# Optimization experiments

Hardware: AMD Instinct MI355X
Metric: run time of the kernel (lower is better)

The kernel has to match this reference:

```python
import jax, jax.numpy as jnp
import numpy as np

B, L, D_MODEL, H, D_QKV = 4, 2048, 1024, 16, 64
SCALE = float(D_MODEL) ** 0.5  # note: source scales by sqrt(d_model), not sqrt(d_qkv)


def setup_inputs() -> dict:
    key = jax.random.key(0)
    ks = jax.random.split(key, 6)
    xavier_qkv = (2.0 / (D_MODEL + D_QKV)) ** 0.5
    xavier_fc = (2.0 / (H * D_QKV + D_MODEL)) ** 0.5
    return {
        "x": jax.random.normal(ks[0], (B, L, D_MODEL), dtype=jnp.float32),
        "mask": jnp.ones((B, L), dtype=jnp.int32),
        "w_q": jax.random.normal(ks[1], (H, D_MODEL, D_QKV), dtype=jnp.float32) * xavier_qkv,
        "w_k": jax.random.normal(ks[2], (H, D_MODEL, D_QKV), dtype=jnp.float32) * xavier_qkv,
        "w_v": jax.random.normal(ks[3], (H, D_MODEL, D_QKV), dtype=jnp.float32) * xavier_qkv,
        "fc_w": jax.random.normal(ks[4], (D_MODEL, H * D_QKV), dtype=jnp.float32) * xavier_fc,
        "fc_b": jnp.zeros((D_MODEL,), dtype=jnp.float32),
    }


def reference(x, mask, w_q, w_k, w_v, fc_w, fc_b):
    # x: [B, L, M]; per-head projections via einsum, as in the source
    q = jnp.einsum('blm,hmd->blhd', x, w_q)
    k = jnp.einsum('blm,hmd->blhd', x, w_k)
    v = jnp.einsum('blm,hmd->blhd', x, w_v)
    scores = jnp.einsum('blhd,bkhd->bhlk', q, k)  # [B, H, L, L]
    m = mask[:, None, None, :]  # unsqueeze(1).unsqueeze(2)
    scores = jnp.where(m == 0, jnp.asarray(-1e9, scores.dtype), scores)
    logits = jax.nn.softmax(scores / SCALE, axis=3)
    # Faithful to source einsum 'bhlk,blhd->blhd' (k is summed out of logits only)
    out = jnp.einsum('bhlk,blhd->blhd', logits, v)
    out = out.reshape(x.shape[0], x.shape[1], H * D_QKV)
    return out @ fc_w.T + fc_b
```

## Files before the change

kernel.cpp:

```cpp
#include <hip/hip_runtime.h>
#include <hip/hip_bf16.h>


typedef __attribute__((ext_vector_type(8))) short bf16x8;
typedef __attribute__((ext_vector_type(4))) float f32x4;

__device__ __forceinline__ f32x4 mfma16(bf16x8 a, bf16x8 b, f32x4 c) {
  return __builtin_amdgcn_mfma_f32_16x16x32_bf16(a, b, c, 0, 0, 0);
}

__device__ __forceinline__ unsigned short f2b(float f) {
  unsigned int u = __builtin_bit_cast(unsigned int, f);
  return (unsigned short)((u + 0x7fffu + ((u >> 16) & 1u)) >> 16);
}

__device__ __forceinline__ bf16x8 cvt8(float4 a, float4 b) {
  bf16x8 r;
  r[0] = (short)f2b(a.x); r[1] = (short)f2b(a.y); r[2] = (short)f2b(a.z); r[3] = (short)f2b(a.w);
  r[4] = (short)f2b(b.x); r[5] = (short)f2b(b.y); r[6] = (short)f2b(b.z); r[7] = (short)f2b(b.w);
  return r;
}

__device__ __forceinline__ void gld_lds16(const void* g, void* l) {
  __builtin_amdgcn_global_load_lds((const __attribute__((address_space(1))) unsigned int*)g,
                                   (__attribute__((address_space(3))) unsigned int*)l, 16, 0, 0);
}

__global__ void cast8(const float* __restrict__ in, unsigned short* __restrict__ out) {
  int i = (blockIdx.x * 256 + threadIdx.x) * 8;
  float4 a = *reinterpret_cast<const float4*>(in + i);
  float4 b = *reinterpret_cast<const float4*>(in + i + 4);
  *reinterpret_cast<bf16x8*>(out + i) = cvt8(a, b);
}

__global__ __launch_bounds__(512) void fold_w(const float* __restrict__ fcw,
                                              const float* __restrict__ wv,
                                              unsigned short* __restrict__ wcT) {
  int wid = threadIdx.x >> 6, lane = threadIdx.x & 63, l16 = lane & 15, quad = lane >> 4;
  int wk = wid >> 2, wr = (wid >> 1) & 1, wc = wid & 1;
  int row0 = blockIdx.y * 64 + wr * 32;
  int col0 = blockIdx.x * 64 + wc * 32;
  f32x4 acc[2][2];
#pragma unroll
  for (int a = 0; a < 2; a++)
#pragma unroll
    for (int b = 0; b < 2; b++) acc[a][b] = (f32x4){0.f, 0.f, 0.f, 0.f};

  for (int k0 = wk * 512; k0 < wk * 512 + 512; k0 += 32) {
    int kk = k0 + quad * 8;
    int h = kk >> 6, d = kk & 63;
    bf16x8 af[2], bfr[2];
#pragma unroll
    for (int rt = 0; rt < 2; rt++) {
      const float* pa = fcw + (row0 + rt * 16 + l16) * 1024 + kk;
      af[rt] = cvt8(*reinterpret_cast<const float4*>(pa), *reinterpret_cast<const float4*>(pa + 4));
    }
#pragma unroll
    for (int ct = 0; ct < 2; ct++) {
      const float* pb = wv + h * 65536 + (col0 + ct * 16 + l16) * 64 + d;
      bfr[ct] = cvt8(*reinterpret_cast<const float4*>(pb), *reinterpret_cast<const float4*>(pb + 4));
    }
#pragma unroll
    for (int rt = 0; rt < 2; rt++)
#pragma unroll
      for (int ct = 0; ct < 2; ct++) acc[rt][ct] = mfma16(af[rt], bfr[ct], acc[rt][ct]);
  }

  __shared__ f32x4 red[4][64][4];
  if (wk == 1) {
#pragma unroll
    for (int rt = 0; rt < 2; rt++)
#pragma unroll
      for (int ct = 0; ct < 2; ct++) red[wid & 3][lane][rt * 2 + ct] = acc[rt][ct];
  }
  __syncthreads();
  if (wk == 0) {
#pragma unroll
    for (int rt = 0; rt < 2; rt++)
#pragma unroll
      for (int ct = 0; ct < 2; ct++) {
        f32x4 s = acc[rt][ct];
        f32x4 o = red[wid & 3][lane][rt * 2 + ct];
        int j0 = row0 + rt * 16 + quad * 4;
        int m = col0 + ct * 16 + l16;
#pragma unroll
        for (int r = 0; r < 4; r++) wcT[(j0 + r) * 1024 + m] = f2b(s[r] + o[r]);
      }
  }
}

__global__ __launch_bounds__(256) void final_gemm(const unsigned short* __restrict__ xb,
                                                  const unsigned short* __restrict__ wcT,
                                                  const float* __restrict__ fcb,
                                                  float* __restrict__ out) {
  __shared__ __align__(16) unsigned short As[2 * 128 * 32];
  __shared__ __align__(16) unsigned short Bs[2 * 128 * 32];
  int t = threadIdx.x, wid = t >> 6, lane = t & 63, l16 = lane & 15, quad = lane >> 4;
  int wr = wid >> 1, wc = wid & 1;
  int row0 = blockIdx.x * 128;
  int col0 = blockIdx.y * 128;

  int w4 = wid * 4;
  const unsigned short* Ap[4];
  const unsigned short* Bp[4];
#pragma unroll
  for (int j = 0; j < 4; j++) {
    int blk = w4 + j;
    int s = blk >> 3, r0 = (blk & 7) * 16;
    int row = r0 + (lane >> 2), kq = lane & 3;
    Ap[j] = xb + (row0 + row) * 1024 + s * 32 + kq * 8;
    Bp[j] = wcT + (col0 + row) * 1024 + s * 32 + kq * 8;
  }

  f32x4 acc[16];
#pragma unroll
  for (int i = 0; i < 16; i++) acc[i] = (f32x4){0.f, 0.f, 0.f, 0.f};

  for (int k0 = 0; k0 < 1024; k0 += 64) {
    __syncthreads();
#pragma unroll
    for (int j = 0; j < 4; j++) {
      int off = (w4 + j) * 512 + lane * 8;
      gld_lds16(Ap[j] + k0, &As[off]);
      gld_lds16(Bp[j] + k0, &Bs[off]);
    }
    __syncthreads();

#pragma unroll
    for (int s = 0; s < 2; s++) {
      bf16x8 af[4], bfr[4];
#pragma unroll
      for (int rt = 0; rt < 4; rt++)
        af[rt] = *reinterpret_cast<const bf16x8*>(&As[s * 4096 + (wr * 64 + rt * 16 + l16) * 32 + quad * 8]);
#pragma unroll
      for (int ct = 0; ct < 4; ct++)
        bfr[ct] = *reinterpret_cast<const bf16x8*>(&Bs[s * 4096 + (wc * 64 + ct * 16 + l16) * 32 + quad * 8]);
#pragma unroll
      for (int rt = 0; rt < 4; rt++)
#pragma unroll
        for (int ct = 0; ct < 4; ct++)
          acc[rt * 4 + ct] = mfma16(af[rt], bfr[ct], acc[rt * 4 + ct]);
    }
  }

#pragma unroll
  for (int ct = 0; ct < 4; ct++) {
    int j = col0 + wc * 64 + ct * 16 + l16;
    float bias = fcb[j];
#pragma unroll
    for (int rt = 0; rt < 4; rt++) {
      int i0 = row0 + wr * 64 + rt * 16 + quad * 4;
      f32x4 a = acc[rt * 4 + ct];
#pragma unroll
      for (int r = 0; r < 4; r++) out[(i0 + r) * 1024 + j] = a[r] + bias;
    }
  }
}

extern "C" void kernel_launch(void* const* d_in, const int* in_sizes, int n_in,
                              void* d_out, int out_size, void* d_ws, size_t ws_size,
                              hipStream_t stream) {
  const float* x   = (const float*)d_in[0];
  const float* wv  = (const float*)d_in[4];
  const float* fcw = (const float*)d_in[5];
  const float* fcb = (const float*)d_in[6];
  float* out = (float*)d_out;

  char* ws = (char*)d_ws;
  unsigned short* xb  = (unsigned short*)(ws);
  unsigned short* wcT = (unsigned short*)(ws + 16777216);

  cast8<<<4096, 256, 0, stream>>>(x, xb);
  fold_w<<<dim3(16, 16), 512, 0, stream>>>(fcw, wv, wcT);
  final_gemm<<<dim3(64, 8), 256, 0, stream>>>(xb, wcT, fcb, out);
}
```

Before: 151.1 us.

## Fuse cast, weight fold and GEMM into one persistent kernel with grid barrier

Merges the three launches into a single 512-block kernel. The first 256 blocks fold fc_w with w_v into the combined weight, using register double-buffered loads and no split-K reduction, while the remaining 256 blocks cast x to bf16. A global atomic barrier then lets every block run its output GEMM tile. This removes two kernel launch gaps and lets the cast and the fold run concurrently. In exchange it adds a memset, a spin barrier that deadlocks if all 512 blocks are not co-resident, and a fold with half the per-block parallelism of before.

```diff
diff --git a/kernel.cpp b/kernel.cpp
--- a/kernel.cpp
+++ b/kernel.cpp
@@ -26,79 +26,99 @@
                                    (__attribute__((address_space(3))) unsigned int*)l, 16, 0, 0);
 }
 
-__global__ void cast8(const float* __restrict__ in, unsigned short* __restrict__ out) {
-  int i = (blockIdx.x * 256 + threadIdx.x) * 8;
-  float4 a = *reinterpret_cast<const float4*>(in + i);
-  float4 b = *reinterpret_cast<const float4*>(in + i + 4);
-  *reinterpret_cast<bf16x8*>(out + i) = cvt8(a, b);
-}
+__global__ __launch_bounds__(256, 2) void fused_all(const float* __restrict__ x,
+                                                    const float* __restrict__ wv,
+                                                    const float* __restrict__ fcw,
+                                                    const float* __restrict__ fcb,
+                                                    unsigned short* __restrict__ xb,
+                                                    unsigned short* __restrict__ wcT,
+                                                    unsigned int* __restrict__ barrier_cnt,
+                                                    float* __restrict__ out) {
+  __shared__ __align__(16) unsigned short As[2 * 128 * 32];
+  __shared__ __align__(16) unsigned short Bs[2 * 128 * 32];
+  int bid = blockIdx.x, t = threadIdx.x;
+  int wid = t >> 6, lane = t & 63, l16 = lane & 15, quad = lane >> 4;
 
-__global__ __launch_bounds__(512) void fold_w(const float* __restrict__ fcw,
-                                              const float* __restrict__ wv,
-                                              unsigned short* __restrict__ wcT) {
-  int wid = threadIdx.x >> 6, lane = threadIdx.x & 63, l16 = lane & 15, quad = lane >> 4;
-  int wk = wid >> 2, wr = (wid >> 1) & 1, wc = wid & 1;
-  int row0 = blockIdx.y * 64 + wr * 32;
-  int col0 = blockIdx.x * 64 + wc * 32;
-  f32x4 acc[2][2];
+  if (bid < 256) {
+    int wr = wid >> 1, wc = wid & 1;
+    int row0 = (bid >> 4) * 64 + wr * 32;
+    int col0 = (bid & 15) * 64 + wc * 32;
+    f32x4 acc[2][2];
 #pragma unroll
-  for (int a = 0; a < 2; a++)
+    for (int a = 0; a < 2; a++)
 #pragma unroll
-    for (int b = 0; b < 2; b++) acc[a][b] = (f32x4){0.f, 0.f, 0.f, 0.f};
+      for (int b = 0; b < 2; b++) acc[a][b] = (f32x4){0.f, 0.f, 0.f, 0.f};
 
-  for (int k0 = wk * 512; k0 < wk * 512 + 512; k0 += 32) {
-    int kk = k0 + quad * 8;
-    int h = kk >> 6, d = kk & 63;
-    bf16x8 af[2], bfr[2];
+    float4 A0[2][2], B0[2][2];
+#define LOADK(kk, Ad, Bd)                                                            \
+    {                                                                                \
+      int h_ = (kk) >> 6, d_ = (kk) & 63;                                            \
+      _Pragma("unroll")                                                              \
+      for (int rt = 0; rt < 2; rt++) {                                               \
+        const float* pa = fcw + (row0 + rt * 16 + l16) * 1024 + (kk);                \
+        Ad[rt][0] = *reinterpret_cast<const float4*>(pa);                            \
+        Ad[rt][1] = *reinterpret_cast<const float4*>(pa + 4);                        \
+      }                                                                              \
+      _Pragma("unroll")                                                              \
+      for (int ct = 0; ct < 2; ct++) {                                               \
+        const float* pb = wv + h_ * 65536 + (col0 + ct * 16 + l16) * 64 + d_;        \
+        Bd[ct][0] = *reinterpret_cast<const float4*>(pb);                            \
+        Bd[ct][1] = *reinterpret_cast<const float4*>(pb + 4);                        \
+      }                                                                              \
+    }
+
+    LOADK(quad * 8, A0, B0);
+    for (int k0 = 0; k0 < 1024; k0 += 32) {
+      float4 A1[2][2], B1[2][2];
+      if (k0 < 992) LOADK(k0 + 32 + quad * 8, A1, B1);
+      bf16x8 af[2], bfr[2];
 #pragma unroll
-    for (int rt = 0; rt < 2; rt++) {
-      const float* pa = fcw + (row0 + rt * 16 + l16) * 1024 + kk;
-      af[rt] = cvt8(*reinterpret_cast<const float4*>(pa), *reinterpret_cast<const float4*>(pa + 4));
+      for (int rt = 0; rt < 2; rt++) af[rt] = cvt8(A0[rt][0], A0[rt][1]);
+#pragma unroll
+      for (int ct = 0; ct < 2; ct++) bfr[ct] = cvt8(B0[ct][0], B0[ct][1]);
+#pragma unroll
+      for (int rt = 0; rt < 2; rt++)
+#pragma unroll
+        for (int ct = 0; ct < 2; ct++) acc[rt][ct] = mfma16(af[rt], bfr[ct], acc[rt][ct]);
+#pragma unroll
+      for (int a = 0; a < 2; a++)
+#pragma unroll
+        for (int b = 0; b < 2; b++) { A0[a][b] = A1[a][b]; B0[a][b] = B1[a][b]; }
     }
-#pragma unroll
-    for (int ct = 0; ct < 2; ct++) {
-      const float* pb = wv + h * 65536 + (col0 + ct * 16 + l16) * 64 + d;
-      bfr[ct] = cvt8(*reinterpret_cast<const float4*>(pb), *reinterpret_cast<const float4*>(pb + 4));
-    }
-#pragma unroll
-    for (int rt = 0; rt < 2; rt++)
-#pragma unroll
-      for (int ct = 0; ct < 2; ct++) acc[rt][ct] = mfma16(af[rt], bfr[ct], acc[rt][ct]);
-  }
-
-  __shared__ f32x4 red[4][64][4];
-  if (wk == 1) {
-#pragma unroll
-    for (int rt = 0; rt < 2; rt++)
-#pragma unroll
-      for (int ct = 0; ct < 2; ct++) red[wid & 3][lane][rt * 2 + ct] = acc[rt][ct];
-  }
-  __syncthreads();
-  if (wk == 0) {
+#undef LOADK
 #pragma unroll
     for (int rt = 0; rt < 2; rt++)
 #pragma unroll
       for (int ct = 0; ct < 2; ct++) {
-        f32x4 s = acc[rt][ct];
-        f32x4 o = red[wid & 3][lane][rt * 2 + ct];
         int j0 = row0 + rt * 16 + quad * 4;
         int m = col0 + ct * 16 + l16;
 #pragma unroll
-        for (int r = 0; r < 4; r++) wcT[(j0 + r) * 1024 + m] = f2b(s[r] + o[r]);
+        for (int r = 0; r < 4; r++) wcT[(j0 + r) * 1024 + m] = f2b(acc[rt][ct][r]);
       }
+  } else {
+    int base0 = (bid - 256) << 15;
+#pragma unroll
+    for (int i = 0; i < 16; i++) {
+      int idx = base0 + i * 2048 + t * 8;
+      float4 a = *reinterpret_cast<const float4*>(x + idx);
+      float4 b = *reinterpret_cast<const float4*>(x + idx + 4);
+      *reinterpret_cast<bf16x8*>(xb + idx) = cvt8(a, b);
+    }
   }
-}
 
-__global__ __launch_bounds__(256) void final_gemm(const unsigned short* __restrict__ xb,
-                                                  const unsigned short* __restrict__ wcT,
-                                                  const float* __restrict__ fcb,
-                                                  float* __restrict__ out) {
-  __shared__ __align__(16) unsigned short As[2 * 128 * 32];
-  __shared__ __align__(16) unsigned short Bs[2 * 128 * 32];
-  int t = threadIdx.x, wid = t >> 6, lane = t & 63, l16 = lane & 15, quad = lane >> 4;
+  __threadfence();
+  __syncthreads();
+  if (t == 0) {
+    __hip_atomic_fetch_add(barrier_cnt, 1u, __ATOMIC_ACQ_REL, __HIP_MEMORY_SCOPE_AGENT);
+    while (__hip_atomic_load(barrier_cnt, __ATOMIC_ACQUIRE, __HIP_MEMORY_SCOPE_AGENT) < 512u)
+      __builtin_amdgcn_s_sleep(8);
+  }
+  __syncthreads();
+  __threadfence();
+
+  int row0 = (bid >> 3) * 128;
+  int col0 = (bid & 7) * 128;
   int wr = wid >> 1, wc = wid & 1;
-  int row0 = blockIdx.x * 128;
-  int col0 = blockIdx.y * 128;
 
   int w4 = wid * 4;
   const unsigned short* Ap[4];
@@ -125,7 +145,6 @@
       gld_lds16(Bp[j] + k0, &Bs[off]);
     }
     __syncthreads();
-
 #pragma unroll
     for (int s = 0; s < 2; s++) {
       bf16x8 af[4], bfr[4];
@@ -169,8 +188,8 @@
   char* ws = (char*)d_ws;
   unsigned short* xb  = (unsigned short*)(ws);
   unsigned short* wcT = (unsigned short*)(ws + 16777216);
+  unsigned int* bar   = (unsigned int*)(ws + 18874368);
 
-  cast8<<<4096, 256, 0, stream>>>(x, xb);
-  fold_w<<<dim3(16, 16), 512, 0, stream>>>(fcw, wv, wcT);
-  final_gemm<<<dim3(64, 8), 256, 0, stream>>>(xb, wcT, fcb, out);
+  hipMemsetAsync(bar, 0, 64, stream);
+  fused_all<<<512, 256, 0, stream>>>(x, wv, fcw, fcb, xb, wcT, bar, out);
 }
```

Result: slower. 376.0 us (+148.9%).
